# Optimization experiments

Measured on AMD Instinct MI355X. Metric: run time of the kernel, lower is better.

## Reference

```python
import jax, jax.numpy as jnp
import numpy as np

N, D = 512, 256          # n candidates, span_emb_size
R = 4                    # num relation types / etypes
FF = 512                 # mention_linker_ffnn_size, depth 1
L = 2                    # ieg_bignn_hidden_layers
DH = D // 2              # GraphConvolution output size


def setup_inputs() -> dict:
    key = jax.random.key(0)
    ks = jax.random.split(key, 12)
    s = lambda fan_in: 1.0 / np.sqrt(fan_in)
    return {
        "candidate_embs": jax.random.normal(ks[0], (N, D), jnp.float32),
        # relation scorer FFNN: 3D -> FF -> R
        "W_sc0": jax.random.normal(ks[1], (3 * D, FF), jnp.float32) * s(3 * D),
        "b_sc0": jnp.zeros((FF,), jnp.float32),
        "W_sc1": jax.random.normal(ks[2], (FF, R), jnp.float32) * s(FF),
        "b_sc1": jnp.zeros((R,), jnp.float32),
        # BiGCN: per-layer, per-relation fw/bw GraphConvolution D -> D//2
        "W_fw": jax.random.normal(ks[3], (L, R, D, DH), jnp.float32) * s(D),
        "b_fw": jnp.zeros((L, R, DH), jnp.float32),
        "W_bw": jax.random.normal(ks[4], (L, R, D, DH), jnp.float32) * s(D),
        "b_bw": jnp.zeros((L, R, DH), jnp.float32),
        # per-layer linear1: D -> D
        "W_lin": jax.random.normal(ks[5], (L, D, D), jnp.float32) * s(D),
        "b_lin": jnp.zeros((L, D), jnp.float32),
    }


def reference(candidate_embs, W_sc0, b_sc0, W_sc1, b_sc1,
              W_fw, b_fw, W_bw, b_bw, W_lin, b_lin):
    n, d = candidate_embs.shape
    # --- get_pair_embs: [n, n, 3d] = cat(src, target, src*target) ---
    src = jnp.broadcast_to(candidate_embs[None, :, :], (n, n, d))   # row i varies j
    tgt = jnp.broadcast_to(candidate_embs[:, None, :], (n, n, d))
    pair = jnp.concatenate([src, tgt, src * tgt], axis=-1)          # [n, n, 3d]
    # --- relation scorer FFNN (ReLU hidden, dropout=0 at inference) ---
    h = jax.nn.relu(jnp.einsum('ijk,kf->ijf', pair, W_sc0) + b_sc0)
    scores = jnp.einsum('ijf,fr->ijr', h, W_sc1) + b_sc1            # [n, n, R]
    probs = jax.nn.softmax(scores, axis=-1)
    # --- adjs_from_preds: detach, zero diagonal; bw = fw^T ---
    probs = jax.lax.stop_gradient(probs)
    A = jnp.moveaxis(probs, -1, 0)                                   # [R, n, n]
    eye = jnp.eye(n, dtype=bool)
    A = jnp.where(eye[None, :, :], 0.0, A)
    AT = jnp.swapaxes(A, 1, 2)
    # --- BiGCN: L layers of multi-relation bi-directional GCN ---
    x = candidate_embs
    for l in range(L):
        sup_fw = jnp.einsum('nd,rde->rne', x, W_fw[l])               # [R, n, DH]
        sup_bw = jnp.einsum('nd,rde->rne', x, W_bw[l])
        fw = jnp.einsum('rij,rje->rie', A, sup_fw) + b_fw[l][:, None, :]
        bw = jnp.einsum('rij,rje->rie', AT, sup_bw) + b_bw[l][:, None, :]
        outs = jnp.concatenate([bw, fw], axis=-1)                    # [R, n, D]
        x = jax.nn.relu(outs.sum(axis=0)) @ W_lin[l] + b_lin[l] + x  # residual
    return x
```

## Files before the change

### kernel.cpp

```cpp
#include <hip/hip_runtime.h>
#include <hip/hip_bf16.h>

using f32x4  = __attribute__((ext_vector_type(4))) float;
using bf16x8 = __attribute__((ext_vector_type(8))) short;

__device__ __forceinline__ unsigned short f2bf(float f) {
    union { __hip_bfloat16 h; unsigned short u; } cv;
    cv.h = __float2bfloat16(f);
    return cv.u;
}
__device__ __forceinline__ unsigned int pack2bf(float lo, float hi) {
    float2 t; t.x = lo; t.y = hi;
    union { __hip_bfloat162 h; unsigned int u; } cv;
    cv.h = __float22bfloat162_rn(t);
    return cv.u;
}
__device__ __forceinline__ float bf2f(unsigned short u) {
    return __uint_as_float((unsigned)u << 16);
}

__global__ __launch_bounds__(512) void prep_uv_kernel(
        const float* __restrict__ E, const float* __restrict__ Wsc0, const float* __restrict__ bsc0,
        const float* __restrict__ Wsc1,
        const float* __restrict__ Wfw, const float* __restrict__ bfw,
        const float* __restrict__ Wbw, const float* __restrict__ bbw,
        const float* __restrict__ Wlin,
        unsigned short* __restrict__ E16, unsigned short* __restrict__ W0p,
        unsigned short* __restrict__ WcatT, unsigned short* __restrict__ WlinT,
        float* __restrict__ bsumS, unsigned short* __restrict__ Upk,
        float* __restrict__ V, unsigned short* __restrict__ W1p) {
    __shared__ float sE[8][256];
    if (blockIdx.x < 512) {
        const int NE = 131072, NW0 = 131072, NCAT = 524288, NLIN = 131072, NW1P = 8192;
        const int total = NE + NW0 + NCAT + NLIN + NW1P + 512;
        for (int idx = blockIdx.x * 512 + threadIdx.x; idx < total; idx += 512 * 512) {
            int t = idx;
            if (t < NE) { E16[t] = f2bf(E[t]); continue; }
            t -= NE;
            if (t < NW0) {
                int e = t & 7, lane = (t >> 3) & 63, kk = (t >> 9) & 7, nb = (t >> 12) & 3, w = (t >> 14) & 7;
                int fcol = w * 64 + nb * 16 + (lane & 15);
                int k = kk * 32 + (lane >> 4) * 8 + e;
                W0p[t] = f2bf(Wsc0[(512 + k) * 512 + fcol]);
                continue;
            }
            t -= NW0;
            if (t < NCAT) {
                int e = t & 127, k = (t >> 7) & 255, r = (t >> 15) & 3, d = (t >> 17) & 1, l = t >> 18;
                const float* src = (d == 0) ? Wfw : Wbw;
                float v = src[((l * 4 + r) * 256 + k) * 128 + e];
                WcatT[(l * 1024 + d * 512 + r * 128 + e) * 256 + k] = f2bf(v);
                continue;
            }
            t -= NCAT;
            if (t < NLIN) {
                int d = t & 255, f = (t >> 8) & 255, l = t >> 16;
                WlinT[(l * 256 + d) * 256 + f] = f2bf(Wlin[(l * 256 + f) * 256 + d]);
                continue;
            }
            t -= NLIN;
            if (t < NW1P) {
                int e = t & 7, lane = (t >> 3) & 63, kk = t >> 9;
                int f = kk * 32 + (lane >> 4) * 8 + e;
                int r = lane & 15;
                W1p[t] = (r < 4) ? f2bf(Wsc1[f * 4 + r]) : (unsigned short)0;
                continue;
            }
            t -= NW1P;
            {
                int f = t & 255, l = t >> 8;
                float s = 0.f;
                if (f < 128) { for (int r = 0; r < 4; ++r) s += bbw[(l * 4 + r) * 128 + f]; }
                else         { for (int r = 0; r < 4; ++r) s += bfw[(l * 4 + r) * 128 + (f - 128)]; }
                bsumS[l * 256 + f] = s;
            }
        }
    } else {
        int j0 = (blockIdx.x - 512) * 8;
        int tid = threadIdx.x;
        for (int t = tid; t < 2048; t += 512) sE[t >> 8][t & 255] = E[j0 * 256 + t];
        __syncthreads();
        int f = tid;
        float u[8] = {0,0,0,0,0,0,0,0}, v[8] = {0,0,0,0,0,0,0,0};
        for (int k = 0; k < 256; ++k) {
            float wa = Wsc0[k * 512 + f];
            float wb = Wsc0[(256 + k) * 512 + f];
#pragma unroll
            for (int jj = 0; jj < 8; ++jj) { u[jj] += sE[jj][k] * wa; v[jj] += sE[jj][k] * wb; }
        }
        float b0f = bsc0[f];
        int w = f >> 6, nb = (f >> 4) & 3, l15 = f & 15;
#pragma unroll
        for (int jj = 0; jj < 8; ++jj) {
            int j = j0 + jj;
            int jt = j >> 6, mb = (j >> 4) & 3, lane = ((j >> 2) & 3) * 16 + l15, reg = j & 3;
            Upk[(((((jt * 8 + w) * 4 + mb) * 4 + nb) * 64 + lane) * 4 + reg)] = f2bf(u[jj] + b0f);
            V[j * 512 + f] = v[jj];
        }
    }
}

__global__ __launch_bounds__(512, 3) void pair_kernel(
    const float* __restrict__ E, const unsigned short* __restrict__ W0p,
    const unsigned short* __restrict__ Upk, const float* __restrict__ V,
    const unsigned short* __restrict__ W1p, const float* __restrict__ b1,
    unsigned short* __restrict__ A16) {

    __shared__ unsigned short prodL[64 * 256];
    __shared__ float Spart[8 * 64 * 5];
    __shared__ float scoresL[64 * 4];

    const int i = blockIdx.x;
    const int jt = blockIdx.y;
    const int j0 = jt * 64;
    const int tid = threadIdx.x;
    const int lane = tid & 63;
    const int w = tid >> 6;
    const int l15 = lane & 15, l4 = lane >> 4;

    float Vv[4];
#pragma unroll
    for (int nb = 0; nb < 4; ++nb) Vv[nb] = V[i * 512 + w * 64 + nb * 16 + l15];
    f32x4 acc[4][4];
#pragma unroll
    for (int mb = 0; mb < 4; ++mb)
#pragma unroll
        for (int nb = 0; nb < 4; ++nb) {
            int idx4 = (((jt * 8 + w) * 4 + mb) * 4 + nb) * 64 + lane;
            ushort4 uq = ((const ushort4*)Upk)[idx4];
            acc[mb][nb][0] = bf2f(uq.x) + Vv[nb];
            acc[mb][nb][1] = bf2f(uq.y) + Vv[nb];
            acc[mb][nb][2] = bf2f(uq.z) + Vv[nb];
            acc[mb][nb][3] = bf2f(uq.w) + Vv[nb];
        }

    {
        int m = tid >> 3;
        const float4* ej = (const float4*)(E + (j0 + m) * 256);
        const float4* ei = (const float4*)(E + i * 256);
        char* base = (char*)prodL;
#pragma unroll
        for (int c = 0; c < 8; ++c) {
            int q = (tid & 7) + c * 8;
            float4 a = ej[q], b = ei[q];
            uint2 val;
            val.x = pack2bf(a.x * b.x, a.y * b.y);
            val.y = pack2bf(a.z * b.z, a.w * b.w);
            int byteoff = m * 512 + ((q * 8) ^ ((m & 7) << 4));
            *(uint2*)(base + byteoff) = val;
        }
    }
    __syncthreads();

    const char* pbase = (const char*)prodL;
    const bf16x8* Wp8 = (const bf16x8*)W0p;
#pragma unroll
    for (int kk = 0; kk < 8; ++kk) {
        bf16x8 afr[4], bfr[4];
#pragma unroll
        for (int mb = 0; mb < 4; ++mb) {
            int row = mb * 16 + l15;
            int off = row * 512 + ((kk * 64 + l4 * 16) ^ ((row & 7) << 4));
            afr[mb] = *(const bf16x8*)(pbase + off);
        }
#pragma unroll
        for (int nb = 0; nb < 4; ++nb)
            bfr[nb] = Wp8[((w * 4 + nb) * 8 + kk) * 64 + lane];
#pragma unroll
        for (int mb = 0; mb < 4; ++mb)
#pragma unroll
            for (int nb = 0; nb < 4; ++nb)
                acc[mb][nb] = __builtin_amdgcn_mfma_f32_16x16x32_bf16(afr[mb], bfr[nb], acc[mb][nb], 0, 0, 0);
    }

    __syncthreads();
    char* hb = (char*)prodL;
    const bf16x8* W1p8 = (const bf16x8*)W1p;
    f32x4 accS[4];
#pragma unroll
    for (int q = 0; q < 4; ++q) accS[q] = (f32x4){0.f, 0.f, 0.f, 0.f};

#pragma unroll
    for (int p = 0; p < 2; ++p) {
#pragma unroll
        for (int mbl = 0; mbl < 2; ++mbl) {
#pragma unroll
            for (int nb = 0; nb < 4; ++nb) {
                int col = w * 64 + nb * 16 + l15;
#pragma unroll
                for (int reg = 0; reg < 4; ++reg) {
                    int rl = mbl * 16 + l4 * 4 + reg;
                    float hv = fmaxf(acc[p * 2 + mbl][nb][reg], 0.f);
                    *(unsigned short*)(hb + rl * 1024 + ((col * 2) ^ ((rl & 7) << 4))) = f2bf(hv);
                }
            }
        }
        __syncthreads();
#pragma unroll
        for (int mbl = 0; mbl < 2; ++mbl) {
            int rl = mbl * 16 + l15;
#pragma unroll
            for (int kkl = 0; kkl < 2; ++kkl) {
                int kk = w * 2 + kkl;
                bf16x8 ha = *(const bf16x8*)(hb + rl * 1024 + ((kk * 64 + l4 * 16) ^ ((rl & 7) << 4)));
                accS[p * 2 + mbl] = __builtin_amdgcn_mfma_f32_16x16x32_bf16(ha, W1p8[kk * 64 + lane], accS[p * 2 + mbl], 0, 0, 0);
            }
        }
        __syncthreads();
    }

    if (l15 < 4) {
#pragma unroll
        for (int q = 0; q < 4; ++q)
#pragma unroll
            for (int reg = 0; reg < 4; ++reg)
                Spart[(w * 64 + q * 16 + l4 * 4 + reg) * 5 + l15] = accS[q][reg];
    }
    __syncthreads();
    if (tid < 256) {
        int m = tid >> 2, r = tid & 3;
        float sc = b1[r];
#pragma unroll
        for (int p8 = 0; p8 < 8; ++p8) sc += Spart[(p8 * 64 + m) * 5 + r];
        scoresL[m * 4 + r] = sc;
    }
    __syncthreads();
    if (tid < 64) {
        int m = tid, j = j0 + m;
        float s0 = scoresL[m * 4 + 0], s1 = scoresL[m * 4 + 1];
        float sA = scoresL[m * 4 + 2], sB = scoresL[m * 4 + 3];
        float mx = fmaxf(fmaxf(s0, s1), fmaxf(sA, sB));
        float e0 = __expf(s0 - mx), e1 = __expf(s1 - mx), e2 = __expf(sA - mx), e3 = __expf(sB - mx);
        float inv = 1.f / (e0 + e1 + e2 + e3);
        float p_[4] = {e0 * inv, e1 * inv, e2 * inv, e3 * inv};
        if (j == i) { p_[0] = p_[1] = p_[2] = p_[3] = 0.f; }
#pragma unroll
        for (int r = 0; r < 4; ++r)
            A16[(r * 512 + i) * 512 + j] = f2bf(p_[r]);
    }
}

template<int K>
__device__ __forceinline__ void stageP(unsigned short* lds, const unsigned short* g, int ldg, int tid) {
    constexpr int SLOTS = K / 8;
#pragma unroll
    for (int it = 0; it < (32 * SLOTS) / 256; ++it) {
        int u = it * 256 + tid;
        int row = u / SLOTS, slot = u % SLOTS;
        uint4 v = *(const uint4*)(g + row * ldg + slot * 8);
        *(uint4*)((char*)lds + row * (K * 2) + ((slot * 16) ^ ((row & 7) << 4))) = v;
    }
}
__device__ __forceinline__ void stage64(unsigned short* lds, const unsigned short* g, int ldg, int tid) {
#pragma unroll
    for (int it = 0; it < 8; ++it) {
        int u = it * 256 + tid;
        int row = u >> 5, slot = u & 31;
        uint4 v = *(const uint4*)(g + row * ldg + slot * 8);
        *(uint4*)((char*)lds + row * 512 + ((slot * 16) ^ ((row & 7) << 4))) = v;
    }
}
template<int K>
__device__ __forceinline__ bf16x8 fragP(const unsigned short* lds, int row, int kc, int l4) {
    return *(const bf16x8*)((const char*)lds + row * (K * 2) + ((((kc * 4 + l4) * 16) ^ ((row & 7) << 4))));
}

__global__ __launch_bounds__(256) void c1_kernel(const unsigned short* __restrict__ WcatT,
                                                 const unsigned short* __restrict__ x16,
                                                 unsigned short* __restrict__ supT,
                                                 const unsigned short* __restrict__ A16,
                                                 unsigned short* __restrict__ AT16, int l) {
    __shared__ unsigned short lA[32 * 256], lB[32 * 256];
    int tid = threadIdx.x;
    if (blockIdx.y >= 16) {
        auto t = (unsigned short(*)[65])lA;
        int job = (blockIdx.y - 16) * 32 + blockIdx.x;
        int r = job >> 6, ty = (job >> 3) & 7, tx = job & 7;
        const unsigned short* src = A16 + (r * 512 + ty * 64) * 512 + tx * 64;
        unsigned short* dst = AT16 + (r * 512 + tx * 64) * 512 + ty * 64;
#pragma unroll
        for (int it = 0; it < 2; ++it) {
            int u = it * 256 + tid, row = u >> 3, c8 = (u & 7) * 8;
            uint4 v = *(const uint4*)(src + row * 512 + c8);
            const unsigned short* p = (const unsigned short*)&v;
#pragma unroll
            for (int e = 0; e < 8; ++e) t[c8 + e][row] = p[e];
        }
        __syncthreads();
#pragma unroll
        for (int it = 0; it < 2; ++it) {
            int u = it * 256 + tid, row = u >> 3, c8 = (u & 7) * 8;
            uint4 v; unsigned short* p = (unsigned short*)&v;
#pragma unroll
            for (int e = 0; e < 8; ++e) p[e] = t[row][c8 + e];
            *(uint4*)(dst + row * 512 + c8) = v;
        }
        return;
    }
    int c0 = blockIdx.x * 32, jt0 = blockIdx.y * 32;
    int lane = tid & 63, w = tid >> 6;
    int wr = (w >> 1) * 16, wc = (w & 1) * 16;
    int l15 = lane & 15, l4 = lane >> 4;
    stageP<256>(lA, WcatT + l * 262144 + c0 * 256, 256, tid);
    stageP<256>(lB, x16 + jt0 * 256, 256, tid);
    __syncthreads();
    f32x4 a0 = {0.f,0.f,0.f,0.f}, a1 = {0.f,0.f,0.f,0.f};
#pragma unroll
    for (int kc = 0; kc < 8; kc += 2) {
        a0 = __builtin_amdgcn_mfma_f32_16x16x32_bf16(fragP<256>(lA, wr + l15, kc, l4),
                                                     fragP<256>(lB, wc + l15, kc, l4), a0, 0, 0, 0);
        a1 = __builtin_amdgcn_mfma_f32_16x16x32_bf16(fragP<256>(lA, wr + l15, kc + 1, l4),
                                                     fragP<256>(lB, wc + l15, kc + 1, l4), a1, 0, 0, 0);
    }
    f32x4 acc = a0 + a1;
#pragma unroll
    for (int reg = 0; reg < 4; ++reg) {
        int c = c0 + wr + l4 * 4 + reg;
        int j = jt0 + wc + l15;
        supT[c * 512 + j] = f2bf(acc[reg]);
    }
}

__global__ __launch_bounds__(256) void c2_kernel(const unsigned short* __restrict__ A16,
                                                 const unsigned short* __restrict__ AT16,
                                                 const unsigned short* __restrict__ supT,
                                                 float* __restrict__ Pc2) {
    __shared__ unsigned short lA[64 * 256], lB[64 * 256];
    int i0 = blockIdx.x * 64, f0 = blockIdx.y * 64;
    int s = blockIdx.z, r = s >> 1, kh = s & 1;
    bool bw = (f0 < 128);
    int e0 = bw ? f0 : (f0 - 128);
    const unsigned short* Am = bw ? AT16 : A16;
    int tid = threadIdx.x, lane = tid & 63, w = tid >> 6;
    int wr = (w >> 1) * 32, wc = (w & 1) * 32;
    int l15 = lane & 15, l4 = lane >> 4;
    stage64(lA, Am + (r * 512 + i0) * 512 + kh * 256, 512, tid);
    stage64(lB, supT + ((bw ? 512 : 0) + r * 128 + e0) * 512 + kh * 256, 512, tid);
    __syncthreads();
    f32x4 acc[2][2];
#pragma unroll
    for (int a_ = 0; a_ < 2; ++a_)
#pragma unroll
        for (int b_ = 0; b_ < 2; ++b_) acc[a_][b_] = (f32x4){0.f, 0.f, 0.f, 0.f};
#pragma unroll
    for (int kc = 0; kc < 8; ++kc) {
        bf16x8 af[2], bf_[2];
#pragma unroll
        for (int mb = 0; mb < 2; ++mb) af[mb] = fragP<256>(lA, wr + mb * 16 + l15, kc, l4);
#pragma unroll
        for (int nb = 0; nb < 2; ++nb) bf_[nb] = fragP<256>(lB, wc + nb * 16 + l15, kc, l4);
#pragma unroll
        for (int mb = 0; mb < 2; ++mb)
#pragma unroll
            for (int nb = 0; nb < 2; ++nb)
                acc[mb][nb] = __builtin_amdgcn_mfma_f32_16x16x32_bf16(af[mb], bf_[nb], acc[mb][nb], 0, 0, 0);
    }
    float* dst = Pc2 + s * 131072;
#pragma unroll
    for (int mb = 0; mb < 2; ++mb)
#pragma unroll
        for (int nb = 0; nb < 2; ++nb)
#pragma unroll
            for (int reg = 0; reg < 4; ++reg)
                dst[(i0 + wr + mb * 16 + l4 * 4 + reg) * 256 + f0 + wc + nb * 16 + l15] = acc[mb][nb][reg];
}

__global__ __launch_bounds__(256) void c3_kernel(const float* __restrict__ Pc2,
                                                 const float* __restrict__ bsumS,
                                                 const unsigned short* __restrict__ WlinT,
                                                 const float* __restrict__ blin,
                                                 const float* __restrict__ xold,
                                                 float* __restrict__ xnew,
                                                 unsigned short* __restrict__ x16out, int l) {
    __shared__ unsigned short lA[32 * 256], lB[32 * 256];
    int i0 = blockIdx.x * 32, d0 = blockIdx.y * 32;
    int tid = threadIdx.x, lane = tid & 63, w = tid >> 6;
    int wr = (w >> 1) * 16, wc = (w & 1) * 16;
    int l15 = lane & 15, l4 = lane >> 4;
#pragma unroll
    for (int g = 0; g < 4; ++g) {
        int u = g * 256 + tid;
        int row = u >> 5, k8 = (u & 31) * 8;
        float s[8] = {0,0,0,0,0,0,0,0};
#pragma unroll
        for (int s8 = 0; s8 < 8; ++s8) {
            const float4* p = (const float4*)(Pc2 + s8 * 131072 + (i0 + row) * 256 + k8);
            float4 a = p[0], b = p[1];
            s[0] += a.x; s[1] += a.y; s[2] += a.z; s[3] += a.w;
            s[4] += b.x; s[5] += b.y; s[6] += b.z; s[7] += b.w;
        }
        uint4 v;
        unsigned* vp = (unsigned*)&v;
#pragma unroll
        for (int e2 = 0; e2 < 4; ++e2) {
            float lo = fmaxf(s[e2 * 2] + bsumS[l * 256 + k8 + e2 * 2], 0.f);
            float hi = fmaxf(s[e2 * 2 + 1] + bsumS[l * 256 + k8 + e2 * 2 + 1], 0.f);
            vp[e2] = pack2bf(lo, hi);
        }
        *(uint4*)((char*)lA + row * 512 + ((k8 * 2) ^ ((row & 7) << 4))) = v;
    }
    stageP<256>(lB, WlinT + l * 65536 + d0 * 256, 256, tid);
    __syncthreads();
    f32x4 a0 = {0.f,0.f,0.f,0.f}, a1 = {0.f,0.f,0.f,0.f};
#pragma unroll
    for (int kc = 0; kc < 8; kc += 2) {
        a0 = __builtin_amdgcn_mfma_f32_16x16x32_bf16(fragP<256>(lA, wr + l15, kc, l4),
                                                     fragP<256>(lB, wc + l15, kc, l4), a0, 0, 0, 0);
        a1 = __builtin_amdgcn_mfma_f32_16x16x32_bf16(fragP<256>(lA, wr + l15, kc + 1, l4),
                                                     fragP<256>(lB, wc + l15, kc + 1, l4), a1, 0, 0, 0);
    }
    f32x4 acc = a0 + a1;
#pragma unroll
    for (int reg = 0; reg < 4; ++reg) {
        int ii = i0 + wr + l4 * 4 + reg;
        int dd = d0 + wc + l15;
        float vv = acc[reg] + blin[l * 256 + dd] + xold[ii * 256 + dd];
        xnew[ii * 256 + dd] = vv;
        x16out[ii * 256 + dd] = f2bf(vv);
    }
}

extern "C" void kernel_launch(void* const* d_in, const int* in_sizes, int n_in,
                              void* d_out, int out_size, void* d_ws, size_t ws_size,
                              hipStream_t stream) {
    const float* E    = (const float*)d_in[0];
    const float* Wsc0 = (const float*)d_in[1];
    const float* bsc0 = (const float*)d_in[2];
    const float* Wsc1 = (const float*)d_in[3];
    const float* bsc1 = (const float*)d_in[4];
    const float* Wfw  = (const float*)d_in[5];
    const float* bfw  = (const float*)d_in[6];
    const float* Wbw  = (const float*)d_in[7];
    const float* bbw  = (const float*)d_in[8];
    const float* Wlin = (const float*)d_in[9];
    const float* blin = (const float*)d_in[10];
    float* out = (float*)d_out;

    char* ws = (char*)d_ws;
    size_t off = 0;
    unsigned short* E16   = (unsigned short*)(ws + off); off += 512 * 256 * 2;
    unsigned short* W0p   = (unsigned short*)(ws + off); off += 512 * 256 * 2;
    unsigned short* WcatT = (unsigned short*)(ws + off); off += 2 * 1024 * 256 * 2;
    unsigned short* WlinT = (unsigned short*)(ws + off); off += 2 * 256 * 256 * 2;
    float* bsumS          = (float*)(ws + off);          off += 2 * 256 * 4;
    unsigned short* Upk   = (unsigned short*)(ws + off); off += 512 * 512 * 2;
    float* V              = (float*)(ws + off);          off += 512 * 512 * 4;
    unsigned short* W1p   = (unsigned short*)(ws + off); off += 16 * 64 * 8 * 2;
    unsigned short* A16   = (unsigned short*)(ws + off); off += 4 * 512 * 512 * 2;
    unsigned short* AT16  = (unsigned short*)(ws + off); off += 4 * 512 * 512 * 2;
    unsigned short* supT  = (unsigned short*)(ws + off); off += 1024 * 512 * 2;
    float* Pc2            = (float*)(ws + off);          off += 8 * 512 * 256 * 4;
    float* xf1            = (float*)(ws + off);          off += 512 * 256 * 4;
    unsigned short* x16_1 = (unsigned short*)(ws + off); off += 512 * 256 * 2;

    prep_uv_kernel<<<576, 512, 0, stream>>>(E, Wsc0, bsc0, Wsc1, Wfw, bfw, Wbw, bbw, Wlin,
                                            E16, W0p, WcatT, WlinT, bsumS, Upk, V, W1p);
    pair_kernel<<<dim3(512, 8), 512, 0, stream>>>(E, W0p, Upk, V, W1p, bsc1, A16);

    for (int l = 0; l < 2; ++l) {
        const unsigned short* xin16 = (l == 0) ? E16 : x16_1;
        const float* xoldf = (l == 0) ? E : xf1;
        float* xout = (l == 0) ? xf1 : out;
        c1_kernel<<<dim3(32, (l == 0) ? 24 : 16), 256, 0, stream>>>(WcatT, xin16, supT, A16, AT16, l);
        c2_kernel<<<dim3(8, 4, 8), 256, 0, stream>>>(A16, AT16, supT, Pc2);
        c3_kernel<<<dim3(16, 8), 256, 0, stream>>>(Pc2, bsumS, WlinT, blin, xoldf, xout, x16_1, l);
    }
    (void)in_sizes; (void)n_in; (void)out_size; (void)ws_size;
}
```

Measured before the change: 212.7 us.

## Compute U/V projections with MFMA in separate kernel and streamline pair epilogue

Splits the scalar-FMA U/V projection out of the prep kernel into a new uv_kernel that uses bf16 MFMA on pre-packed Wsc0 halves, storing V transposed in bf16 instead of fp32. In pair_kernel the hidden-layer write to LDS is vectorized (packed bf16 pairs, with W1p reordered to match), W1 fragments are hoisted into registers, and the Spart cross-wave reduction is replaced by LDS atomicAdd into bias-initialized scores. It also drops the occupancy hint of 3 blocks per CU. The intent is to cut the slow scalar prep path and reduce LDS traffic and synchronization in the pair epilogue. It costs an extra kernel launch that runs on only 16 blocks, and V is now rounded to bf16.

```diff
diff --git a/kernel.cpp b/kernel.cpp
--- a/kernel.cpp
+++ b/kernel.cpp
@@ -19,95 +19,145 @@
     return __uint_as_float((unsigned)u << 16);
 }
 
-__global__ __launch_bounds__(512) void prep_uv_kernel(
-        const float* __restrict__ E, const float* __restrict__ Wsc0, const float* __restrict__ bsc0,
-        const float* __restrict__ Wsc1,
+__global__ __launch_bounds__(512) void prep_kernel(
+        const float* __restrict__ E, const float* __restrict__ Wsc0, const float* __restrict__ Wsc1,
         const float* __restrict__ Wfw, const float* __restrict__ bfw,
         const float* __restrict__ Wbw, const float* __restrict__ bbw,
         const float* __restrict__ Wlin,
         unsigned short* __restrict__ E16, unsigned short* __restrict__ W0p,
+        unsigned short* __restrict__ WabP,
         unsigned short* __restrict__ WcatT, unsigned short* __restrict__ WlinT,
-        float* __restrict__ bsumS, unsigned short* __restrict__ Upk,
-        float* __restrict__ V, unsigned short* __restrict__ W1p) {
-    __shared__ float sE[8][256];
-    if (blockIdx.x < 512) {
-        const int NE = 131072, NW0 = 131072, NCAT = 524288, NLIN = 131072, NW1P = 8192;
-        const int total = NE + NW0 + NCAT + NLIN + NW1P + 512;
-        for (int idx = blockIdx.x * 512 + threadIdx.x; idx < total; idx += 512 * 512) {
-            int t = idx;
-            if (t < NE) { E16[t] = f2bf(E[t]); continue; }
-            t -= NE;
-            if (t < NW0) {
-                int e = t & 7, lane = (t >> 3) & 63, kk = (t >> 9) & 7, nb = (t >> 12) & 3, w = (t >> 14) & 7;
-                int fcol = w * 64 + nb * 16 + (lane & 15);
-                int k = kk * 32 + (lane >> 4) * 8 + e;
-                W0p[t] = f2bf(Wsc0[(512 + k) * 512 + fcol]);
-                continue;
+        float* __restrict__ bsumS, unsigned short* __restrict__ W1p) {
+    const int NE = 131072, NW0 = 131072, NWAB = 262144, NCAT = 524288, NLIN = 131072, NW1P = 8192;
+    const int total = NE + NW0 + NWAB + NCAT + NLIN + NW1P + 512;
+    for (int idx = blockIdx.x * 512 + threadIdx.x; idx < total; idx += 512 * 512) {
+        int t = idx;
+        if (t < NE) { E16[t] = f2bf(E[t]); continue; }
+        t -= NE;
+        if (t < NW0) {
+            int e = t & 7, lane = (t >> 3) & 63, kk = (t >> 9) & 7, nb = (t >> 12) & 3, w = (t >> 14) & 7;
+            int fcol = w * 64 + nb * 16 + (lane & 15);
+            int k = kk * 32 + (lane >> 4) * 8 + e;
+            W0p[t] = f2bf(Wsc0[(512 + k) * 512 + fcol]);
+            continue;
+        }
+        t -= NW0;
+        if (t < NWAB) {
+            int e = t & 7, lane = (t >> 3) & 63, kk = (t >> 9) & 7, nb = (t >> 12) & 3, wf = t >> 14;
+            int fcol = wf * 64 + nb * 16 + (lane & 15);
+            int k = kk * 32 + (lane >> 4) * 8 + e;
+            int row = (fcol < 512) ? k : (256 + k);
+            WabP[t] = f2bf(Wsc0[row * 512 + (fcol & 511)]);
+            continue;
+        }
+        t -= NWAB;
+        if (t < NCAT) {
+            int e = t & 127, k = (t >> 7) & 255, r = (t >> 15) & 3, d = (t >> 17) & 1, l = t >> 18;
+            const float* src = (d == 0) ? Wfw : Wbw;
+            float v = src[((l * 4 + r) * 256 + k) * 128 + e];
+            WcatT[(l * 1024 + d * 512 + r * 128 + e) * 256 + k] = f2bf(v);
+            continue;
+        }
+        t -= NCAT;
+        if (t < NLIN) {
+            int d = t & 255, f = (t >> 8) & 255, l = t >> 16;
+            WlinT[(l * 256 + d) * 256 + f] = f2bf(Wlin[(l * 256 + f) * 256 + d]);
+            continue;
+        }
+        t -= NLIN;
+        if (t < NW1P) {
+            int e = t & 7, lane = (t >> 3) & 63, kap = t >> 9;
+            int fp = kap * 32 + (lane >> 4) * 8 + e;
+            int w = fp >> 6, q = (fp >> 2) & 15, nb = fp & 3;
+            int f = w * 64 + nb * 16 + q;
+            int r = lane & 15;
+            W1p[t] = (r < 4) ? f2bf(Wsc1[f * 4 + r]) : (unsigned short)0;
+            continue;
+        }
+        t -= NW1P;
+        {
+            int f = t & 255, l = t >> 8;
+            float s = 0.f;
+            if (f < 128) { for (int r = 0; r < 4; ++r) s += bbw[(l * 4 + r) * 128 + f]; }
+            else         { for (int r = 0; r < 4; ++r) s += bfw[(l * 4 + r) * 128 + (f - 128)]; }
+            bsumS[l * 256 + f] = s;
+        }
+    }
+}
+
+__global__ __launch_bounds__(512) void uv_kernel(const unsigned short* __restrict__ E16,
+                                                 const unsigned short* __restrict__ WabP,
+                                                 const float* __restrict__ bsc0,
+                                                 unsigned short* __restrict__ Upk,
+                                                 unsigned short* __restrict__ VT16) {
+    __shared__ unsigned short sE[32 * 256];
+    const int jt = blockIdx.x;
+    const int tid = threadIdx.x, lane = tid & 63, w = tid >> 6;
+    const int l15 = lane & 15, l4 = lane >> 4;
+#pragma unroll
+    for (int it = 0; it < 2; ++it) {
+        int u = it * 512 + tid;
+        int row = u >> 5, slot = u & 31;
+        uint4 v = *(const uint4*)(E16 + (jt * 32 + row) * 256 + slot * 8);
+        *(uint4*)((char*)sE + row * 512 + ((slot * 16) ^ ((row & 7) << 4))) = v;
+    }
+    __syncthreads();
+    const bf16x8* Wab8 = (const bf16x8*)WabP;
+    f32x4 acc[2][8];
+#pragma unroll
+    for (int a_ = 0; a_ < 2; ++a_)
+#pragma unroll
+        for (int b_ = 0; b_ < 8; ++b_) acc[a_][b_] = (f32x4){0.f, 0.f, 0.f, 0.f};
+#pragma unroll
+    for (int kk = 0; kk < 8; ++kk) {
+        bf16x8 af[2];
+#pragma unroll
+        for (int mbl = 0; mbl < 2; ++mbl) {
+            int row = mbl * 16 + l15;
+            af[mbl] = *(const bf16x8*)((char*)sE + row * 512 + ((kk * 64 + l4 * 16) ^ ((row & 7) << 4)));
+        }
+#pragma unroll
+        for (int nb = 0; nb < 8; ++nb) {
+            int wf = 2 * w + (nb >> 2);
+            bf16x8 bfr = Wab8[((wf * 4 + (nb & 3)) * 8 + kk) * 64 + lane];
+#pragma unroll
+            for (int mbl = 0; mbl < 2; ++mbl)
+                acc[mbl][nb] = __builtin_amdgcn_mfma_f32_16x16x32_bf16(af[mbl], bfr, acc[mbl][nb], 0, 0, 0);
+        }
+    }
+#pragma unroll
+    for (int mbl = 0; mbl < 2; ++mbl) {
+        int j_base = jt * 32 + mbl * 16 + l4 * 4;
+#pragma unroll
+        for (int nb = 0; nb < 8; ++nb) {
+            int f_g = (2 * w + (nb >> 2)) * 64 + (nb & 3) * 16 + l15;
+            ushort4 o;
+            if (f_g < 512) {
+                float b0f = bsc0[f_g];
+                o.x = f2bf(acc[mbl][nb][0] + b0f);
+                o.y = f2bf(acc[mbl][nb][1] + b0f);
+                o.z = f2bf(acc[mbl][nb][2] + b0f);
+                o.w = f2bf(acc[mbl][nb][3] + b0f);
+                int idx = (((j_base >> 6) * 8 + (f_g >> 6)) * 4 + ((j_base >> 4) & 3)) * 4 + ((f_g >> 4) & 3);
+                *(ushort4*)(Upk + (idx * 64 + (l4 * 16 + l15)) * 4) = o;
+            } else {
+                o.x = f2bf(acc[mbl][nb][0]);
+                o.y = f2bf(acc[mbl][nb][1]);
+                o.z = f2bf(acc[mbl][nb][2]);
+                o.w = f2bf(acc[mbl][nb][3]);
+                *(ushort4*)(VT16 + (f_g - 512) * 512 + j_base) = o;
             }
-            t -= NW0;
-            if (t < NCAT) {
-                int e = t & 127, k = (t >> 7) & 255, r = (t >> 15) & 3, d = (t >> 17) & 1, l = t >> 18;
-                const float* src = (d == 0) ? Wfw : Wbw;
-                float v = src[((l * 4 + r) * 256 + k) * 128 + e];
-                WcatT[(l * 1024 + d * 512 + r * 128 + e) * 256 + k] = f2bf(v);
-                continue;
-            }
-            t -= NCAT;
-            if (t < NLIN) {
-                int d = t & 255, f = (t >> 8) & 255, l = t >> 16;
-                WlinT[(l * 256 + d) * 256 + f] = f2bf(Wlin[(l * 256 + f) * 256 + d]);
-                continue;
-            }
-            t -= NLIN;
-            if (t < NW1P) {
-                int e = t & 7, lane = (t >> 3) & 63, kk = t >> 9;
-                int f = kk * 32 + (lane >> 4) * 8 + e;
-                int r = lane & 15;
-                W1p[t] = (r < 4) ? f2bf(Wsc1[f * 4 + r]) : (unsigned short)0;
-                continue;
-            }
-            t -= NW1P;
-            {
-                int f = t & 255, l = t >> 8;
-                float s = 0.f;
-                if (f < 128) { for (int r = 0; r < 4; ++r) s += bbw[(l * 4 + r) * 128 + f]; }
-                else         { for (int r = 0; r < 4; ++r) s += bfw[(l * 4 + r) * 128 + (f - 128)]; }
-                bsumS[l * 256 + f] = s;
-            }
-        }
-    } else {
-        int j0 = (blockIdx.x - 512) * 8;
-        int tid = threadIdx.x;
-        for (int t = tid; t < 2048; t += 512) sE[t >> 8][t & 255] = E[j0 * 256 + t];
-        __syncthreads();
-        int f = tid;
-        float u[8] = {0,0,0,0,0,0,0,0}, v[8] = {0,0,0,0,0,0,0,0};
-        for (int k = 0; k < 256; ++k) {
-            float wa = Wsc0[k * 512 + f];
-            float wb = Wsc0[(256 + k) * 512 + f];
-#pragma unroll
-            for (int jj = 0; jj < 8; ++jj) { u[jj] += sE[jj][k] * wa; v[jj] += sE[jj][k] * wb; }
-        }
-        float b0f = bsc0[f];
-        int w = f >> 6, nb = (f >> 4) & 3, l15 = f & 15;
-#pragma unroll
-        for (int jj = 0; jj < 8; ++jj) {
-            int j = j0 + jj;
-            int jt = j >> 6, mb = (j >> 4) & 3, lane = ((j >> 2) & 3) * 16 + l15, reg = j & 3;
-            Upk[(((((jt * 8 + w) * 4 + mb) * 4 + nb) * 64 + lane) * 4 + reg)] = f2bf(u[jj] + b0f);
-            V[j * 512 + f] = v[jj];
-        }
-    }
-}
-
-__global__ __launch_bounds__(512, 3) void pair_kernel(
+        }
+    }
+}
+
+__global__ __launch_bounds__(512) void pair_kernel(
     const float* __restrict__ E, const unsigned short* __restrict__ W0p,
-    const unsigned short* __restrict__ Upk, const float* __restrict__ V,
+    const unsigned short* __restrict__ Upk, const unsigned short* __restrict__ VT16,
     const unsigned short* __restrict__ W1p, const float* __restrict__ b1,
     unsigned short* __restrict__ A16) {
 
     __shared__ unsigned short prodL[64 * 256];
-    __shared__ float Spart[8 * 64 * 5];
     __shared__ float scoresL[64 * 4];
 
     const int i = blockIdx.x;
@@ -120,7 +170,7 @@
 
     float Vv[4];
 #pragma unroll
-    for (int nb = 0; nb < 4; ++nb) Vv[nb] = V[i * 512 + w * 64 + nb * 16 + l15];
+    for (int nb = 0; nb < 4; ++nb) Vv[nb] = bf2f(VT16[(w * 64 + nb * 16 + l15) * 512 + i]);
     f32x4 acc[4][4];
 #pragma unroll
     for (int mb = 0; mb < 4; ++mb)
@@ -173,9 +223,15 @@
                 acc[mb][nb] = __builtin_amdgcn_mfma_f32_16x16x32_bf16(afr[mb], bfr[nb], acc[mb][nb], 0, 0, 0);
     }
 
-    __syncthreads();
+    if (tid < 256) scoresL[tid] = b1[tid & 3];
+    __syncthreads();
+
     char* hb = (char*)prodL;
     const bf16x8* W1p8 = (const bf16x8*)W1p;
+    bf16x8 w1f[2];
+#pragma unroll
+    for (int kl = 0; kl < 2; ++kl) w1f[kl] = W1p8[(w * 2 + kl) * 64 + lane];
+
     f32x4 accS[4];
 #pragma unroll
     for (int q = 0; q < 4; ++q) accS[q] = (f32x4){0.f, 0.f, 0.f, 0.f};
@@ -184,15 +240,18 @@
     for (int p = 0; p < 2; ++p) {
 #pragma unroll
         for (int mbl = 0; mbl < 2; ++mbl) {
-#pragma unroll
-            for (int nb = 0; nb < 4; ++nb) {
-                int col = w * 64 + nb * 16 + l15;
-#pragma unroll
-                for (int reg = 0; reg < 4; ++reg) {
-                    int rl = mbl * 16 + l4 * 4 + reg;
-                    float hv = fmaxf(acc[p * 2 + mbl][nb][reg], 0.f);
-                    *(unsigned short*)(hb + rl * 1024 + ((col * 2) ^ ((rl & 7) << 4))) = f2bf(hv);
-                }
+            int mb = p * 2 + mbl;
+#pragma unroll
+            for (int reg = 0; reg < 4; ++reg) {
+                int rl = mbl * 16 + l4 * 4 + reg;
+                float h0 = fmaxf(acc[mb][0][reg], 0.f);
+                float h1 = fmaxf(acc[mb][1][reg], 0.f);
+                float h2 = fmaxf(acc[mb][2][reg], 0.f);
+                float h3 = fmaxf(acc[mb][3][reg], 0.f);
+                uint2 val;
+                val.x = pack2bf(h0, h1);
+                val.y = pack2bf(h2, h3);
+                *(uint2*)(hb + rl * 1024 + ((w * 128 + l15 * 8) ^ ((rl & 7) << 4))) = val;
             }
         }
         __syncthreads();
@@ -200,10 +259,9 @@
         for (int mbl = 0; mbl < 2; ++mbl) {
             int rl = mbl * 16 + l15;
 #pragma unroll
-            for (int kkl = 0; kkl < 2; ++kkl) {
-                int kk = w * 2 + kkl;
-                bf16x8 ha = *(const bf16x8*)(hb + rl * 1024 + ((kk * 64 + l4 * 16) ^ ((rl & 7) << 4)));
-                accS[p * 2 + mbl] = __builtin_amdgcn_mfma_f32_16x16x32_bf16(ha, W1p8[kk * 64 + lane], accS[p * 2 + mbl], 0, 0, 0);
+            for (int kl = 0; kl < 2; ++kl) {
+                bf16x8 ha = *(const bf16x8*)(hb + rl * 1024 + (((w * 2 + kl) * 64 + l4 * 16) ^ ((rl & 7) << 4)));
+                accS[p * 2 + mbl] = __builtin_amdgcn_mfma_f32_16x16x32_bf16(ha, w1f[kl], accS[p * 2 + mbl], 0, 0, 0);
             }
         }
         __syncthreads();
@@ -214,15 +272,7 @@
         for (int q = 0; q < 4; ++q)
 #pragma unroll
             for (int reg = 0; reg < 4; ++reg)
-                Spart[(w * 64 + q * 16 + l4 * 4 + reg) * 5 + l15] = accS[q][reg];
-    }
-    __syncthreads();
-    if (tid < 256) {
-        int m = tid >> 2, r = tid & 3;
-        float sc = b1[r];
-#pragma unroll
-        for (int p8 = 0; p8 < 8; ++p8) sc += Spart[(p8 * 64 + m) * 5 + r];
-        scoresL[m * 4 + r] = sc;
+                atomicAdd(&scoresL[(q * 16 + l4 * 4 + reg) * 4 + l15], accS[q][reg]);
     }
     __syncthreads();
     if (tid < 64) {
@@ -440,11 +490,12 @@
     size_t off = 0;
     unsigned short* E16   = (unsigned short*)(ws + off); off += 512 * 256 * 2;
     unsigned short* W0p   = (unsigned short*)(ws + off); off += 512 * 256 * 2;
+    unsigned short* WabP  = (unsigned short*)(ws + off); off += 1024 * 256 * 2;
     unsigned short* WcatT = (unsigned short*)(ws + off); off += 2 * 1024 * 256 * 2;
     unsigned short* WlinT = (unsigned short*)(ws + off); off += 2 * 256 * 256 * 2;
     float* bsumS          = (float*)(ws + off);          off += 2 * 256 * 4;
     unsigned short* Upk   = (unsigned short*)(ws + off); off += 512 * 512 * 2;
-    float* V              = (float*)(ws + off);          off += 512 * 512 * 4;
+    unsigned short* VT16  = (unsigned short*)(ws + off); off += 512 * 512 * 2;
     unsigned short* W1p   = (unsigned short*)(ws + off); off += 16 * 64 * 8 * 2;
     unsigned short* A16   = (unsigned short*)(ws + off); off += 4 * 512 * 512 * 2;
     unsigned short* AT16  = (unsigned short*)(ws + off); off += 4 * 512 * 512 * 2;
@@ -453,9 +504,10 @@
     float* xf1            = (float*)(ws + off);          off += 512 * 256 * 4;
     unsigned short* x16_1 = (unsigned short*)(ws + off); off += 512 * 256 * 2;
 
-    prep_uv_kernel<<<576, 512, 0, stream>>>(E, Wsc0, bsc0, Wsc1, Wfw, bfw, Wbw, bbw, Wlin,
-                                            E16, W0p, WcatT, WlinT, bsumS, Upk, V, W1p);
-    pair_kernel<<<dim3(512, 8), 512, 0, stream>>>(E, W0p, Upk, V, W1p, bsc1, A16);
+    prep_kernel<<<512, 512, 0, stream>>>(E, Wsc0, Wsc1, Wfw, bfw, Wbw, bbw, Wlin,
+                                         E16, W0p, WabP, WcatT, WlinT, bsumS, W1p);
+    uv_kernel<<<16, 512, 0, stream>>>(E16, WabP, bsc0, Upk, VT16);
+    pair_kernel<<<dim3(512, 8), 512, 0, stream>>>(E, W0p, Upk, VT16, W1p, bsc1, A16);
 
     for (int l = 0; l < 2; ++l) {
         const unsigned short* xin16 = (l == 0) ? E16 : x16_1;
```

Result: faster. 199.6 us (-6.2%).
